# Kernel optimization log

Measured on AMD Instinct MI355X. Metric: run time of the kernel, lower is better.

The kernel has to match this reference:

```python
import jax, jax.numpy as jnp
import numpy as np

# Hard-coded dims from MambaLayer.__init__
D_IN = 20        # input feature dim (Dense infers it; chosen = modelInternalDim)
D_INNER = 20     # modelInternalDim
N_STATES = 10    # modelStates
DT_RANK = 5      # delta_t_rank
BATCH = 4
SEQ = 32768


def setup_inputs() -> dict:
    key = jax.random.key(0)
    ks = jax.random.split(key, 8)
    s = lambda k, shape: jax.random.normal(k, shape, dtype=jnp.float32) * 0.05
    A = jnp.tile(jnp.arange(1, N_STATES + 1, dtype=jnp.float32)[None, :], (D_INNER, 1))
    return {
        "x": jax.random.normal(ks[0], (BATCH, SEQ, D_IN), dtype=jnp.float32),
        "w_in": s(ks[1], (D_IN, 2 * D_INNER)),
        "b_in": jnp.zeros((2 * D_INNER,), jnp.float32),
        "conv_k": s(ks[2], (3, D_INNER, D_INNER)),   # (W, I, O)
        "conv_b": jnp.zeros((D_INNER,), jnp.float32),
        "w_x": s(ks[3], (D_INNER, DT_RANK + 2 * N_STATES)),
        "b_x": jnp.zeros((DT_RANK + 2 * N_STATES,), jnp.float32),
        "w_dt": s(ks[4], (DT_RANK, D_INNER)),
        "b_dt": jnp.zeros((D_INNER,), jnp.float32),
        "A_log": jnp.log(A),
        "D_param": jnp.ones((D_INNER,), jnp.float32),
    }


def _selective_scan(u, delta, A, B, C, D):
    # u, delta: (b,l,d); A: (d,n); B, C: (b,l,n); D: (d,)
    dA = jnp.einsum('bld,dn->bldn', delta, A)                  # (b,l,d,n)
    dB_u = jnp.einsum('bld,bld,bln->bldn', delta, u, B)        # (b,l,d,n)
    # tf.pad(dA[:,1:], [[0,0],[1,1],...])[:,1:] == concat(dA[:,1:], zeros) along l
    dA_shift = jnp.concatenate([dA[:, 1:], jnp.zeros_like(dA[:, :1])], axis=1)
    # reversed cumsum, exponentiate, reverse back
    dA_cumsum = jnp.exp(jnp.flip(jnp.cumsum(jnp.flip(dA_shift, axis=1), axis=1), axis=1))
    x = jnp.cumsum(dB_u * dA_cumsum, axis=1) / (dA_cumsum + 1e-12)
    y = jnp.einsum('bldn,bln->bld', x, C)
    return y + u * D


def reference(x, w_in, b_in, conv_k, conv_b, w_x, b_x, w_dt, b_dt, A_log, D_param):
    # in_projection + split (res half is unused, matching the original call())
    h = x @ w_in + b_in                                        # (b,l,2d)
    h, _res = jnp.split(h, 2, axis=-1)
    # causal Conv1D, kernel_size=3: left-pad by 2
    h = jax.lax.conv_general_dilated(
        h, conv_k, window_strides=(1,), padding=[(2, 0)],
        dimension_numbers=('NWC', 'WIO', 'NWC')) + conv_b
    h = jax.nn.silu(h)                                         # tf.nn.swish
    # ssm
    A = -jnp.exp(A_log)                                        # (d,n)
    xp = h @ w_x + b_x                                         # (b,l,r+2n)
    delta = xp[..., :DT_RANK]
    Bm = xp[..., DT_RANK:DT_RANK + N_STATES]
    Cm = xp[..., DT_RANK + N_STATES:]
    delta = jax.nn.softmax(delta @ w_dt + b_dt, axis=-1)       # (b,l,d)
    return _selective_scan(h, delta, A, Bm, Cm, D_param)
```

## Files before the change

### kernel.cpp

```cpp
#include <hip/hip_runtime.h>
#include <math.h>

#define B_   4
#define L_   32768
#define DI   20
#define NS   10
#define TBLK 128
#define NCB  256

#define OFF_AP   0u
#define OFF_RS   204800u
#define OFF_SC   409600u
#define OFF_TOT  430080u
#define OFF_H16  430192u
#define HD  0u
#define HU  2621440u
#define HB  5242880u
#define HC  6553600u

typedef _Float16 h16;
typedef _Float16 half8 __attribute__((ext_vector_type(8)));
typedef _Float16 half4 __attribute__((ext_vector_type(4)));
typedef float f32x4 __attribute__((ext_vector_type(4)));

template<int CTRL>
__device__ __forceinline__ float dppf(float idv, float src) {
    union U { float f; int i; };
    U o, s, r; o.f = idv; s.f = src;
    r.i = __builtin_amdgcn_update_dpp(o.i, s.i, CTRL, 0xf, 0xf, false);
    return r.f;
}
#define ROW_SHR1 0x111
#define ROW_SHR2 0x112
#define ROW_SHR4 0x114
#define ROW_SHR8 0x118

#define OPSCAN16(Ac, Bc) \
    { float aP = dppf<ROW_SHR1>(1.0f, Ac); float bP = dppf<ROW_SHR1>(0.0f, Bc); \
      Bc = fmaf(Ac, bP, Bc); Ac *= aP; \
      aP = dppf<ROW_SHR2>(1.0f, Ac); bP = dppf<ROW_SHR2>(0.0f, Bc); \
      Bc = fmaf(Ac, bP, Bc); Ac *= aP; \
      aP = dppf<ROW_SHR4>(1.0f, Ac); bP = dppf<ROW_SHR4>(0.0f, Bc); \
      Bc = fmaf(Ac, bP, Bc); Ac *= aP; \
      aP = dppf<ROW_SHR8>(1.0f, Ac); bP = dppf<ROW_SHR8>(0.0f, Bc); \
      Bc = fmaf(Ac, bP, Bc); Ac *= aP; }

#define SUMSCAN16(v) \
    { v += dppf<ROW_SHR1>(0.0f, v); v += dppf<ROW_SHR2>(0.0f, v); \
      v += dppf<ROW_SHR4>(0.0f, v); v += dppf<ROW_SHR8>(0.0f, v); }

#define XS_   0
#define MT_   2640
#define UL_   0
#define DS__  0
#define DUS_  2720
#define XP5_  4608
#define BS_   5448
#define WXo   6808
#define WDTo  7808
#define BDTo  7908
#define BXo   7928
#define POOLH 7956
#define WF_   7956
#define POOL2 (POOLH + 3200)

__global__ __launch_bounds__(320) void k1(
    const float* __restrict__ x,
    const float* __restrict__ w_in, const float* __restrict__ b_in,
    const float* __restrict__ conv_k, const float* __restrict__ conv_b,
    const float* __restrict__ w_x, const float* __restrict__ b_x,
    const float* __restrict__ w_dt, const float* __restrict__ b_dt,
    const float* __restrict__ A_log,
    h16* __restrict__ dh, h16* __restrict__ uh,
    h16* __restrict__ Bh, h16* __restrict__ Ch,
    float* __restrict__ ap_ws, float* __restrict__ rs_ws, float* __restrict__ sc_ws)
{
    __shared__ __align__(16) h16 P[POOL2];
    __shared__ float beff_s[20];
    __shared__ float ALs[200];

    const int tid = threadIdx.x;
    const int c   = blockIdx.x;
    const int b   = blockIdx.y;
    const int l0  = c * TBLK;

    {
        float* Wf = (float*)&P[WF_];
        for (int i = tid; i < 400;  i += 320) Wf[i]       = w_in[(i/20)*40 + (i%20)];
        for (int i = tid; i < 1200; i += 320) Wf[400 + i] = conv_k[i];
        for (int i = tid; i < 200;  i += 320) ALs[i] = -__expf(A_log[i]);
    }
    __syncthreads();

    {
        const float* Wf = (const float*)&P[WF_];
        for (int e = tid; e < 1200; e += 320) {
            int cc = e/20, o = e - cc*20;
            int w = cc/20, i = cc - w*20;
            float acc = 0.0f;
            #pragma unroll
            for (int op = 0; op < 20; op++)
                acc = fmaf(Wf[i*20 + op], Wf[400 + (w*20 + op)*20 + o], acc);
            P[MT_ + o*72 + cc] = (h16)acc;
        }
        for (int i = tid; i < 240; i += 320) {
            int o = i/12, cc = 60 + (i - (i/12)*12);
            P[MT_ + o*72 + cc] = (h16)0.0f;
        }
        for (int i = tid; i < 1000; i += 320) {
            int j = i/40, k = i - j*40;
            P[WXo + i] = (k < 20) ? (h16)w_x[k*25 + j] : (h16)0.0f;
        }
        for (int i = tid; i < 100; i += 320) P[WDTo + i] = (h16)w_dt[i];
        if (tid < 20) P[BDTo + tid] = (h16)b_dt[tid];
        if (tid < 25) P[BXo + tid] = (h16)b_x[tid];
        if (tid < 20) {
            float be = conv_b[tid];
            #pragma unroll
            for (int w = 0; w < 3; w++)
                #pragma unroll
                for (int op = 0; op < 20; op++)
                    be = fmaf(b_in[op], Wf[400 + (w*20 + op)*20 + tid], be);
            beff_s[tid] = be;
        }
        const float* xb = x + ((size_t)b*L_ + l0)*DI - 2*DI;
        for (int i = tid; i < 1320; i += 320) {
            float2 v;
            if (i >= 1300 || (c == 0 && i < 20)) v = make_float2(0.0f, 0.0f);
            else v = *(const float2*)(xb + 2*i);
            P[XS_ + 2*i]     = (h16)v.x;
            P[XS_ + 2*i + 1] = (h16)v.y;
        }
    }
    __syncthreads();

    const int wv  = tid >> 6;
    const int ln  = tid & 63;
    const int m16 = ln & 15;
    const int q   = ln >> 4;
    float uval[4][4];
    if (wv < 4) {
        #pragma unroll
        for (int jj = 0; jj < 4; jj++) {
            int job = wv*4 + jj, mt = job >> 1, nt = job & 1;
            int t_row = mt*16 + m16;
            int dcol  = nt*16 + m16;
            int dmin  = dcol < 20 ? dcol : 19;
            f32x4 acc = {0.0f, 0.0f, 0.0f, 0.0f};
            #pragma unroll
            for (int kh = 0; kh < 2; kh++) {
                half8 af, bf;
                int ab = XS_ + t_row*20 + kh*32 + (q<<3);
                *(half4*)&af         = *(const half4*)&P[ab];
                *(((half4*)&af) + 1) = *(const half4*)&P[ab + 4];
                int bb = MT_ + dmin*72 + kh*32 + (q<<3);
                *(half4*)&bf         = *(const half4*)&P[bb];
                *(((half4*)&bf) + 1) = *(const half4*)&P[bb + 4];
                acc = __builtin_amdgcn_mfma_f32_16x16x32_f16(af, bf, acc, 0, 0, 0);
            }
            float bfv = beff_s[dmin];
            #pragma unroll
            for (int r = 0; r < 4; r++) {
                float a = acc[r] + bfv;
                uval[jj][r] = a * __builtin_amdgcn_rcpf(1.0f + __expf(-a));
            }
        }
    }
    __syncthreads();

    if (wv < 4) {
        #pragma unroll
        for (int jj = 0; jj < 4; jj++) {
            int job = wv*4 + jj, mt = job >> 1, nt = job & 1;
            int dcol = nt*16 + m16;
            if (dcol < 20) {
                #pragma unroll
                for (int r = 0; r < 4; r++)
                    P[UL_ + (mt*16 + q*4 + r)*36 + dcol] = (h16)uval[jj][r];
            }
        }
    }
    __syncthreads();

    float xv[4][4];
    if (wv < 4) {
        #pragma unroll
        for (int jj = 0; jj < 4; jj++) {
            int job = wv*4 + jj, mt = job >> 1, nt = job & 1;
            int t_row = mt*16 + m16;
            int j     = nt*16 + m16;
            int jmin  = j < 25 ? j : 24;
            f32x4 acc = {0.0f, 0.0f, 0.0f, 0.0f};
            half8 af, bf;
            int ab = UL_ + t_row*36 + (q<<3);
            *(half4*)&af         = *(const half4*)&P[ab];
            *(((half4*)&af) + 1) = *(const half4*)&P[ab + 4];
            int bb = WXo + jmin*40 + (q<<3);
            *(half4*)&bf         = *(const half4*)&P[bb];
            *(((half4*)&bf) + 1) = *(const half4*)&P[bb + 4];
            acc = __builtin_amdgcn_mfma_f32_16x16x32_f16(af, bf, acc, 0, 0, 0);
            float bx = (j < 25) ? (float)P[BXo + j] : 0.0f;
            #pragma unroll
            for (int r = 0; r < 4; r++) xv[jj][r] = acc[r] + bx;
        }
        #pragma unroll
        for (int jj = 0; jj < 4; jj++) {
            int job = wv*4 + jj, mt = job >> 1, nt = job & 1;
            int j = nt*16 + m16;
            #pragma unroll
            for (int r = 0; r < 4; r++) {
                int t = mt*16 + q*4 + r;
                h16 hv = (h16)xv[jj][r];
                if (j < 5)       P[XP5_ + t*5 + j] = hv;
                else if (j < 15) P[BS_ + (j - 5)*136 + t] = hv;
                else if (j < 25) Ch[(size_t)(b*NS + (j - 15))*L_ + l0 + t] = hv;
            }
        }
    }
    __syncthreads();

    h16 urow[20];
    float dl[20];
    if (tid < 128) {
        const int t = tid;
        *(half4*)&urow[0]  = *(const half4*)&P[UL_ + t*36 + 0];
        *(half4*)&urow[4]  = *(const half4*)&P[UL_ + t*36 + 4];
        *(half4*)&urow[8]  = *(const half4*)&P[UL_ + t*36 + 8];
        *(half4*)&urow[12] = *(const half4*)&P[UL_ + t*36 + 12];
        *(half4*)&urow[16] = *(const half4*)&P[UL_ + t*36 + 16];
        #pragma unroll
        for (int d2 = 0; d2 < 20; d2++)
            uh[(size_t)(b*DI + d2)*L_ + l0 + t] = urow[d2];
        #pragma unroll
        for (int n = 0; n < NS; n++)
            Bh[(size_t)(b*NS + n)*L_ + l0 + t] = P[BS_ + n*136 + t];
        float xq[5];
        #pragma unroll
        for (int r = 0; r < 5; r++) xq[r] = (float)P[XP5_ + t*5 + r];
        #pragma unroll
        for (int d2 = 0; d2 < 20; d2++) dl[d2] = (float)P[BDTo + d2];
        #pragma unroll
        for (int r = 0; r < 5; r++) {
            float dv = xq[r];
            #pragma unroll
            for (int d2 = 0; d2 < 20; d2++)
                dl[d2] = fmaf(dv, (float)P[WDTo + r*20 + d2], dl[d2]);
        }
        float mx = dl[0];
        #pragma unroll
        for (int d2 = 1; d2 < 20; d2++) mx = fmaxf(mx, dl[d2]);
        float sm = 0.0f;
        #pragma unroll
        for (int d2 = 0; d2 < 20; d2++) { dl[d2] = __expf(dl[d2] - mx); sm += dl[d2]; }
        float inv = __builtin_amdgcn_rcpf(sm);
        #pragma unroll
        for (int d2 = 0; d2 < 20; d2++) dl[d2] *= inv;
    }
    __syncthreads();

    if (tid < 128) {
        const int t = tid;
        #pragma unroll
        for (int d2 = 0; d2 < 20; d2++) {
            h16 dlh = (h16)dl[d2];
            P[DS__ + d2*136 + t] = dlh;
            P[DUS_ + d2*136 + t] = (h16)((float)dlh * (float)urow[d2]);
            dh[(size_t)(b*DI + d2)*L_ + l0 + t] = dlh;
        }
    }
    __syncthreads();

    const int d  = tid >> 4;
    const int s  = tid & 15;
    const int bd = b*DI + d;

    float d8[8], du8[8];
    { half8 hv = *(const half8*)&P[DS__ + d*136 + 8*s];
      #pragma unroll
      for (int j = 0; j < 8; j++) d8[j] = (float)hv[j]; }
    { half8 hv = *(const half8*)&P[DUS_ + d*136 + 8*s];
      #pragma unroll
      for (int j = 0; j < 8; j++) du8[j] = (float)hv[j]; }

    float ssum = 0.0f;
    #pragma unroll
    for (int j = 0; j < 8; j++) ssum += d8[j];
    SUMSCAN16(ssum);
    if (s == 15) sc_ws[(size_t)bd*NCB + c] = ssum;

    float A_dn[NS];
    #pragma unroll
    for (int n = 0; n < NS; n++) A_dn[n] = ALs[d*NS + n];

    float AcA[NS], BcA[NS];
    #pragma unroll
    for (int n = 0; n < NS; n++) {
        half8 bv = *(const half8*)&P[BS_ + n*136 + 8*s];
        float Ac = 1.0f, Bc = 0.0f;
        #pragma unroll
        for (int j = 0; j < 8; j++) {
            float a = __expf(A_dn[n]*d8[j]);
            Bc = fmaf(a, Bc, du8[j]*(float)bv[j]);
            Ac *= a;
        }
        AcA[n] = Ac; BcA[n] = Bc;
    }
    #pragma unroll
    for (int n = 0; n < NS; n++) { OPSCAN16(AcA[n], BcA[n]); }
    if (s == 15) {
        const size_t o0 = ((size_t)bd*NS)*NCB + c;
        #pragma unroll
        for (int n = 0; n < NS; n++) {
            ap_ws[o0 + (size_t)n*NCB] = AcA[n];
            rs_ws[o0 + (size_t)n*NCB] = BcA[n];
        }
    }
}

__global__ __launch_bounds__(64) void kC2(
    const float* __restrict__ ap_ws, float* __restrict__ rs_ws,
    float* __restrict__ sc_ws, float* __restrict__ tot_ws)
{
    const int bd   = blockIdx.x;
    const int lane = threadIdx.x;
    const size_t sb = (size_t)bd*NCB + lane*4;

    float4 sv = *(const float4*)(sc_ws + sb);
    float l1 = sv.x, l2 = l1 + sv.y, l3 = l2 + sv.z, l4 = l3 + sv.w;
    float inc = l4;
    #pragma unroll
    for (int off = 1; off < 64; off <<= 1) {
        float t = __shfl_up(inc, off);
        if (lane >= off) inc += t;
    }
    float ex = __shfl_up(inc, 1);
    if (lane == 0) ex = 0.0f;
    *(float4*)(sc_ws + sb) = make_float4(ex, ex + l1, ex + l2, ex + l3);
    if (lane == 63) tot_ws[bd] = inc;

    #pragma unroll 2
    for (int n = 0; n < NS; n++) {
        const size_t base = ((size_t)bd*NS + n)*NCB + lane*4;
        float4 av = *(const float4*)(ap_ws + base);
        float4 rv = *(const float4*)(rs_ws + base);
        float Ac = av.x, Bc = rv.x;
        Bc = fmaf(av.y, Bc, rv.y); Ac *= av.y;
        Bc = fmaf(av.z, Bc, rv.z); Ac *= av.z;
        Bc = fmaf(av.w, Bc, rv.w); Ac *= av.w;
        #pragma unroll
        for (int off = 1; off < 64; off <<= 1) {
            float aP = __shfl_up(Ac, off);
            float bP = __shfl_up(Bc, off);
            if (lane >= off) { Bc = fmaf(Ac, bP, Bc); Ac *= aP; }
        }
        float pB = __shfl_up(Bc, 1);
        if (lane == 0) pB = 0.0f;
        float r  = pB;
        float o0 = r; r = fmaf(av.x, r, rv.x);
        float o1 = r; r = fmaf(av.y, r, rv.y);
        float o2 = r; r = fmaf(av.z, r, rv.z);
        float o3 = r;
        *(float4*)(rs_ws + base) = make_float4(o0, o1, o2, o3);
    }
}

__global__ __launch_bounds__(320) void kD(
    const h16* __restrict__ dh, const h16* __restrict__ uh,
    const h16* __restrict__ Bh, const h16* __restrict__ Ch,
    const float* __restrict__ A_log, const float* __restrict__ D_param,
    const float* __restrict__ rs_ws, const float* __restrict__ sc_ws,
    const float* __restrict__ tot_ws, float* __restrict__ out)
{
    __shared__ float ylT[20*132];
    const int tid = threadIdx.x;
    const int d   = tid >> 4;
    const int s   = tid & 15;
    const int c   = blockIdx.x;
    const int b   = blockIdx.y;
    const int bd  = b*DI + d;
    const size_t t0 = (size_t)c*TBLK + s*8;

    const float Tot = tot_ws[bd];
    float A_dn[NS];
    float Amax = -1e30f;
    #pragma unroll
    for (int n = 0; n < NS; n++) {
        A_dn[n] = -__expf(A_log[d*NS + n]);
        Amax = fmaxf(Amax, A_dn[n]);
    }
    const float pref_end = (c + 1 < NCB) ? sc_ws[(size_t)bd*NCB + c + 1] : Tot;
    const bool active = fmaf(Amax, Tot - pref_end, 40.0f) > 0.0f;

    float u8[8];
    { half8 hv = *(const half8*)(uh + (size_t)bd*L_ + t0);
      #pragma unroll
      for (int j = 0; j < 8; j++) u8[j] = (float)hv[j]; }
    const float Dd = D_param[d];
    float yv[8];
    #pragma unroll
    for (int j = 0; j < 8; j++) yv[j] = u8[j]*Dd;

    if (active) {
        float d8[8], du8[8];
        { half8 hv = *(const half8*)(dh + (size_t)bd*L_ + t0);
          #pragma unroll
          for (int j = 0; j < 8; j++) d8[j] = (float)hv[j]; }
        #pragma unroll
        for (int j = 0; j < 8; j++) du8[j] = d8[j]*u8[j];

        float lp[8];
        { float run = 0.0f;
          #pragma unroll
          for (int j = 0; j < 8; j++) { run += d8[j]; lp[j] = run; } }
        float inc = lp[7];
        SUMSCAN16(inc);
        float ex = dppf<ROW_SHR1>(0.0f, inc);
        const float basep = sc_ws[(size_t)bd*NCB + c] + ex;

        float rin[NS];
        #pragma unroll
        for (int n = 0; n < NS; n++) rin[n] = rs_ws[((size_t)bd*NS + n)*NCB + c];

        float yacc[8];
        #pragma unroll
        for (int j = 0; j < 8; j++) yacc[j] = 0.0f;

        #pragma unroll 2
        for (int n = 0; n < NS; n++) {
            half8 bv = *(const half8*)(Bh + (size_t)(b*NS + n)*L_ + t0);
            half8 cv = *(const half8*)(Ch + (size_t)(b*NS + n)*L_ + t0);
            float a8[8], b8[8];
            #pragma unroll
            for (int j = 0; j < 8; j++) {
                a8[j] = __expf(A_dn[n]*d8[j]);
                b8[j] = du8[j]*(float)bv[j];
            }
            float Ac = 1.0f, Bc = 0.0f;
            #pragma unroll
            for (int j = 0; j < 8; j++) { Bc = fmaf(a8[j], Bc, b8[j]); Ac *= a8[j]; }
            OPSCAN16(Ac, Bc);
            float pA = dppf<ROW_SHR1>(1.0f, Ac);
            float pB = dppf<ROW_SHR1>(0.0f, Bc);
            float r  = fmaf(pA, rin[n], pB);

            float G[8];
            G[7] = __expf(A_dn[n]*(Tot - (basep + lp[7])));
            #pragma unroll
            for (int j = 6; j >= 0; j--) G[j] = G[j+1]*a8[j+1];
            #pragma unroll
            for (int j = 0; j < 8; j++) {
                r = fmaf(a8[j], r, b8[j]);
                float damp = G[j] * __builtin_amdgcn_rcpf(G[j] + 1e-12f);
                yacc[j] = fmaf((float)cv[j]*damp, r, yacc[j]);
            }
        }
        #pragma unroll
        for (int j = 0; j < 8; j++) yv[j] = fmaf(u8[j], Dd, yacc[j]);
    }

    *(float4*)&ylT[d*132 + 8*s]     = *(float4*)(yv);
    *(float4*)&ylT[d*132 + 8*s + 4] = *(float4*)(yv + 4);
    __syncthreads();

    float4* ob4 = (float4*)(out + ((size_t)b*L_ + (size_t)c*TBLK)*DI);
    for (int i = tid; i < TBLK*DI/4; i += 320) {
        int t = i / 5, qq = (i - t*5)*4;
        ob4[i] = make_float4(ylT[qq*132 + t], ylT[(qq+1)*132 + t],
                             ylT[(qq+2)*132 + t], ylT[(qq+3)*132 + t]);
    }
}

extern "C" void kernel_launch(void* const* d_in, const int* in_sizes, int n_in,
                              void* d_out, int out_size, void* d_ws, size_t ws_size,
                              hipStream_t stream) {
    const float* x      = (const float*)d_in[0];
    const float* w_in   = (const float*)d_in[1];
    const float* b_in   = (const float*)d_in[2];
    const float* conv_k = (const float*)d_in[3];
    const float* conv_b = (const float*)d_in[4];
    const float* w_x    = (const float*)d_in[5];
    const float* b_x    = (const float*)d_in[6];
    const float* w_dt   = (const float*)d_in[7];
    const float* b_dt   = (const float*)d_in[8];
    const float* A_log  = (const float*)d_in[9];
    const float* D_par  = (const float*)d_in[10];
    float* out = (float*)d_out;
    float* ws  = (float*)d_ws;

    float* ap_ws  = ws + OFF_AP;
    float* rs_ws  = ws + OFF_RS;
    float* sc_ws  = ws + OFF_SC;
    float* tot_ws = ws + OFF_TOT;
    h16*   hbase  = (h16*)(ws + OFF_H16);
    h16* dh  = hbase + HD;
    h16* uh  = hbase + HU;
    h16* Bh  = hbase + HB;
    h16* Ch  = hbase + HC;

    k1<<<dim3(NCB, B_), 320, 0, stream>>>(x, w_in, b_in, conv_k, conv_b,
                                          w_x, b_x, w_dt, b_dt, A_log,
                                          dh, uh, Bh, Ch,
                                          ap_ws, rs_ws, sc_ws);
    kC2<<<B_*DI, 64, 0, stream>>>(ap_ws, rs_ws, sc_ws, tot_ws);
    kD<<<dim3(NCB, B_), 320, 0, stream>>>(dh, uh, Bh, Ch, A_log, D_par,
                                          rs_ws, sc_ws, tot_ws, out);
}
```

Measured before the change: 120.6 us.

## Fold chunk-carry scan into final kernel, removing the middle scan launch

Removes the kC2 kernel that computed exclusive prefix sums of delta and the chunk-carry recurrence across chunks. Instead, each kD block recomputes the delta prefix sum with a 16-lane reduction over its row, and lanes s<10 serially fold the preceding chunk carries (a loop over c chunks) to get its incoming state. This saves one kernel launch and the workspace round-trip, at the cost of O(c) redundant serial work per block, up to 255 dependent FMAs with global loads for late chunks.

```diff
diff --git a/kernel.cpp b/kernel.cpp
--- a/kernel.cpp
+++ b/kernel.cpp
@@ -11,7 +11,6 @@
 #define OFF_AP   0u
 #define OFF_RS   204800u
 #define OFF_SC   409600u
-#define OFF_TOT  430080u
 #define OFF_H16  430192u
 #define HD  0u
 #define HU  2621440u
@@ -317,70 +316,23 @@
     }
 }
 
-__global__ __launch_bounds__(64) void kC2(
-    const float* __restrict__ ap_ws, float* __restrict__ rs_ws,
-    float* __restrict__ sc_ws, float* __restrict__ tot_ws)
-{
-    const int bd   = blockIdx.x;
-    const int lane = threadIdx.x;
-    const size_t sb = (size_t)bd*NCB + lane*4;
-
-    float4 sv = *(const float4*)(sc_ws + sb);
-    float l1 = sv.x, l2 = l1 + sv.y, l3 = l2 + sv.z, l4 = l3 + sv.w;
-    float inc = l4;
-    #pragma unroll
-    for (int off = 1; off < 64; off <<= 1) {
-        float t = __shfl_up(inc, off);
-        if (lane >= off) inc += t;
-    }
-    float ex = __shfl_up(inc, 1);
-    if (lane == 0) ex = 0.0f;
-    *(float4*)(sc_ws + sb) = make_float4(ex, ex + l1, ex + l2, ex + l3);
-    if (lane == 63) tot_ws[bd] = inc;
-
-    #pragma unroll 2
-    for (int n = 0; n < NS; n++) {
-        const size_t base = ((size_t)bd*NS + n)*NCB + lane*4;
-        float4 av = *(const float4*)(ap_ws + base);
-        float4 rv = *(const float4*)(rs_ws + base);
-        float Ac = av.x, Bc = rv.x;
-        Bc = fmaf(av.y, Bc, rv.y); Ac *= av.y;
-        Bc = fmaf(av.z, Bc, rv.z); Ac *= av.z;
-        Bc = fmaf(av.w, Bc, rv.w); Ac *= av.w;
-        #pragma unroll
-        for (int off = 1; off < 64; off <<= 1) {
-            float aP = __shfl_up(Ac, off);
-            float bP = __shfl_up(Bc, off);
-            if (lane >= off) { Bc = fmaf(Ac, bP, Bc); Ac *= aP; }
-        }
-        float pB = __shfl_up(Bc, 1);
-        if (lane == 0) pB = 0.0f;
-        float r  = pB;
-        float o0 = r; r = fmaf(av.x, r, rv.x);
-        float o1 = r; r = fmaf(av.y, r, rv.y);
-        float o2 = r; r = fmaf(av.z, r, rv.z);
-        float o3 = r;
-        *(float4*)(rs_ws + base) = make_float4(o0, o1, o2, o3);
-    }
-}
-
 __global__ __launch_bounds__(320) void kD(
     const h16* __restrict__ dh, const h16* __restrict__ uh,
     const h16* __restrict__ Bh, const h16* __restrict__ Ch,
     const float* __restrict__ A_log, const float* __restrict__ D_param,
-    const float* __restrict__ rs_ws, const float* __restrict__ sc_ws,
-    const float* __restrict__ tot_ws, float* __restrict__ out)
+    const float* __restrict__ ap_ws, const float* __restrict__ rs_ws,
+    const float* __restrict__ sc_ws, float* __restrict__ out)
 {
     __shared__ float ylT[20*132];
     const int tid = threadIdx.x;
     const int d   = tid >> 4;
     const int s   = tid & 15;
+    const int lnw = tid & 63;
     const int c   = blockIdx.x;
     const int b   = blockIdx.y;
     const int bd  = b*DI + d;
     const size_t t0 = (size_t)c*TBLK + s*8;
 
-    const float Tot = tot_ws[bd];
     float A_dn[NS];
     float Amax = -1e30f;
     #pragma unroll
@@ -388,7 +340,25 @@
         A_dn[n] = -__expf(A_log[d*NS + n]);
         Amax = fmaxf(Amax, A_dn[n]);
     }
-    const float pref_end = (c + 1 < NCB) ? sc_ws[(size_t)bd*NCB + c + 1] : Tot;
+
+    float totp = 0.0f, clipp = 0.0f;
+    {
+        const float4* sc4 = (const float4*)(sc_ws + (size_t)bd*NCB + s*16);
+        #pragma unroll
+        for (int q4 = 0; q4 < 4; q4++) {
+            float4 v = sc4[q4];
+            int base = s*16 + q4*4;
+            totp  += v.x + v.y + v.z + v.w;
+            clipp += (base + 0 < c ? v.x : 0.0f) + (base + 1 < c ? v.y : 0.0f)
+                   + (base + 2 < c ? v.z : 0.0f) + (base + 3 < c ? v.w : 0.0f);
+        }
+    }
+    SUMSCAN16(totp);
+    SUMSCAN16(clipp);
+    const float Tot = __shfl(totp,  lnw | 15);
+    const float Pc  = __shfl(clipp, lnw | 15);
+    const float sc_c = sc_ws[(size_t)bd*NCB + c];
+    const float pref_end = Pc + sc_c;
     const bool active = fmaf(Amax, Tot - pref_end, 40.0f) > 0.0f;
 
     float u8[8];
@@ -401,6 +371,18 @@
     for (int j = 0; j < 8; j++) yv[j] = u8[j]*Dd;
 
     if (active) {
+        float rser = 0.0f;
+        if (s < NS) {
+            const float* aprow = ap_ws + ((size_t)bd*NS + s)*NCB;
+            const float* rsrow = rs_ws + ((size_t)bd*NS + s)*NCB;
+            #pragma unroll 4
+            for (int c2 = 0; c2 < c; c2++)
+                rser = fmaf(aprow[c2], rser, rsrow[c2]);
+        }
+        float rin[NS];
+        #pragma unroll
+        for (int n = 0; n < NS; n++) rin[n] = __shfl(rser, (lnw & 48) | n);
+
         float d8[8], du8[8];
         { half8 hv = *(const half8*)(dh + (size_t)bd*L_ + t0);
           #pragma unroll
@@ -415,11 +397,7 @@
         float inc = lp[7];
         SUMSCAN16(inc);
         float ex = dppf<ROW_SHR1>(0.0f, inc);
-        const float basep = sc_ws[(size_t)bd*NCB + c] + ex;
-
-        float rin[NS];
-        #pragma unroll
-        for (int n = 0; n < NS; n++) rin[n] = rs_ws[((size_t)bd*NS + n)*NCB + c];
+        const float basep = Pc + ex;
 
         float yacc[8];
         #pragma unroll
@@ -490,7 +468,6 @@
     float* ap_ws  = ws + OFF_AP;
     float* rs_ws  = ws + OFF_RS;
     float* sc_ws  = ws + OFF_SC;
-    float* tot_ws = ws + OFF_TOT;
     h16*   hbase  = (h16*)(ws + OFF_H16);
     h16* dh  = hbase + HD;
     h16* uh  = hbase + HU;
@@ -501,7 +478,6 @@
                                           w_x, b_x, w_dt, b_dt, A_log,
                                           dh, uh, Bh, Ch,
                                           ap_ws, rs_ws, sc_ws);
-    kC2<<<B_*DI, 64, 0, stream>>>(ap_ws, rs_ws, sc_ws, tot_ws);
     kD<<<dim3(NCB, B_), 320, 0, stream>>>(dh, uh, Bh, Ch, A_log, D_par,
-                                          rs_ws, sc_ws, tot_ws, out);
+                                          ap_ws, rs_ws, sc_ws, out);
 }
```

Result: slower. 131.8 us (+9.3%).
